# Performance work log

Hardware: AMD Instinct MI355X
Metric: run time of the kernel (lower is better)

The kernel has to match this reference:

```python
import jax, jax.numpy as jnp
import numpy as np

B, N, D, H, MLP_H = 4, 2048, 256, 8, 1024
E = 262144
DH = D // H
EPS = 1e-5

def _ln(x, g, b):
    mu = jnp.mean(x, axis=-1, keepdims=True)
    var = jnp.mean((x - mu) ** 2, axis=-1, keepdims=True)
    return (x - mu) * jax.lax.rsqrt(var + EPS) * g + b

def setup_inputs() -> dict:
    key = jax.random.key(0)
    ks = jax.random.split(key, 16)
    s = 0.02
    return {
        "x": jax.random.normal(ks[0], (B, N, D), jnp.float32),
        "edge_index": jax.random.randint(ks[1], (2, E), 0, B * N, dtype=jnp.int64),
        "gc_w": jax.random.normal(ks[2], (D, D), jnp.float32) * s,
        "gc_b": jnp.zeros((D,), jnp.float32),
        "g_gamma": jnp.ones((D,), jnp.float32), "g_beta": jnp.zeros((D,), jnp.float32),
        "wq": jax.random.normal(ks[3], (D, D), jnp.float32) * s, "bq": jnp.zeros((D,), jnp.float32),
        "wk": jax.random.normal(ks[4], (D, D), jnp.float32) * s, "bk": jnp.zeros((D,), jnp.float32),
        "wv": jax.random.normal(ks[5], (D, D), jnp.float32) * s, "bv": jnp.zeros((D,), jnp.float32),
        "wo": jax.random.normal(ks[6], (D, D), jnp.float32) * s, "bo": jnp.zeros((D,), jnp.float32),
        "a_gamma": jnp.ones((D,), jnp.float32), "a_beta": jnp.zeros((D,), jnp.float32),
        "w1": jax.random.normal(ks[7], (D, MLP_H), jnp.float32) * s, "b1": jnp.zeros((MLP_H,), jnp.float32),
        "w2": jax.random.normal(ks[8], (MLP_H, D), jnp.float32) * s, "b2": jnp.zeros((D,), jnp.float32),
        "m_gamma": jnp.ones((D,), jnp.float32), "m_beta": jnp.zeros((D,), jnp.float32),
    }

def reference(x, edge_index, gc_w, gc_b, g_gamma, g_beta,
              wq, bq, wk, bk, wv, bv, wo, bo, a_gamma, a_beta,
              w1, b1, w2, b2, m_gamma, m_beta):
    BN = B * N
    row, col = edge_index[0], edge_index[1]
    # GraphConvolution with symmetric degree normalization
    xf = x.reshape(BN, D)
    xt = xf @ gc_w  # [BN, D]
    deg = jax.ops.segment_sum(jnp.ones((E,), x.dtype), row, num_segments=BN)
    dis = jnp.where(deg > 0, deg ** -0.5, 0.0)  # deg^-0.5, inf -> 0
    norm = dis[row] * dis[col]  # [E]
    out = jax.ops.segment_sum(norm[:, None] * xt[row], col, num_segments=BN) + gc_b
    x = _ln(x + out.reshape(B, N, D), g_gamma, g_beta)
    # Multi-head self-attention (no mask, dropout=0)
    q = (x @ wq + bq).reshape(B, N, H, DH)
    k = (x @ wk + bk).reshape(B, N, H, DH)
    v = (x @ wv + bv).reshape(B, N, H, DH)
    scores = jnp.einsum("bqhd,bkhd->bhqk", q, k) / jnp.sqrt(jnp.float32(DH))
    attn = jax.nn.softmax(scores, axis=-1)
    ao = jnp.einsum("bhqk,bkhd->bqhd", attn, v).reshape(B, N, D) @ wo + bo
    x = _ln(x + ao, a_gamma, a_beta)
    # MLP (GELU exact, dropout inactive at eval)
    h = jax.nn.gelu(x @ w1 + b1, approximate=False)
    x = _ln(x + (h @ w2 + b2), m_gamma, m_beta)
    return x
```

## Files before the change

kernel.cpp:

```cpp
#include <hip/hip_runtime.h>
#include <math.h>

#define Bb 4
#define Nn 2048
#define Dd 256
#define Hh 8
#define DHh 32
#define MLPH 1024
#define Ee 262144
#define BNr 8192
#define KS_S 40
#define VT_S 72
#define PS 72

typedef __attribute__((ext_vector_type(8))) short bf8;
typedef __attribute__((ext_vector_type(4))) float f4;

__device__ __forceinline__ float gelu_f(float x){
  return 0.5f * x * (1.0f + erff(x * 0.70710678118654752f));
}

__device__ __forceinline__ ushort f2bf(float f){
  union { float f; unsigned u; } v; v.f = f;
  unsigned r = v.u + 0x7fffu + ((v.u >> 16) & 1u);
  return (ushort)(r >> 16);
}
__device__ __forceinline__ float bf2f(ushort u){
  return __uint_as_float((unsigned)u << 16);
}

__global__ void detect_kernel(const int* __restrict__ ei, int* flag){
  __shared__ int nz;
  if (threadIdx.x == 0) nz = 0;
  __syncthreads();
  int any = 0;
  for (int i = threadIdx.x; i < 2048; i += 256)
    if (ei[2*i + 1] != 0) any = 1;
  if (any) atomicOr(&nz, 1);
  __syncthreads();
  if (threadIdx.x == 0) *flag = nz ? 0 : 1;
}

__global__ void count_kernel(const int* __restrict__ ei, const int* __restrict__ flag,
                             int* cnt_row, int* cnt_col){
  int e = blockIdx.x * 256 + threadIdx.x;
  if (e >= Ee) return;
  int m = *flag;
  int r = m ? ei[2*e]          : ei[e];
  int c = m ? ei[2*(Ee + e)]   : ei[Ee + e];
  atomicAdd(&cnt_row[r], 1);
  atomicAdd(&cnt_col[c], 1);
}

__global__ void scan_kernel(const int* __restrict__ cnt, const int* __restrict__ cnt_row,
                            int* start, int* cursor, float* dis){
  __shared__ int part[256];
  int t = threadIdx.x;
  int s = 0;
  for (int i = 0; i < 32; i++) s += cnt[t*32 + i];
  part[t] = s;
  __syncthreads();
  if (t == 0){
    int run = 0;
    for (int i = 0; i < 256; i++){ int tmp = part[i]; part[i] = run; run += tmp; }
    start[BNr] = run;
  }
  __syncthreads();
  int base = part[t];
  for (int i = 0; i < 32; i++){
    start[t*32 + i]  = base;
    cursor[t*32 + i] = base;
    base += cnt[t*32 + i];
  }
  for (int i = t; i < BNr; i += 256){
    int d = cnt_row[i];
    dis[i] = d > 0 ? 1.0f / sqrtf((float)d) : 0.0f;
  }
}

__global__ void fill_kernel(const int* __restrict__ ei, const int* __restrict__ flag,
                            const float* __restrict__ dis,
                            int* cursor, int* bucketR, float* bucketN){
  int e = blockIdx.x * 256 + threadIdx.x;
  if (e >= Ee) return;
  int m = *flag;
  int r = m ? ei[2*e]        : ei[e];
  int c = m ? ei[2*(Ee + e)] : ei[Ee + e];
  int p = atomicAdd(&cursor[c], 1);
  bucketR[p] = r;
  bucketN[p] = dis[r] * dis[c];
}

__global__ void conv_kernel(const float* __restrict__ src, ushort* __restrict__ dst, int n4){
  int i = blockIdx.x * 256 + threadIdx.x;
  if (i < n4){
    float4 v = ((const float4*)src)[i];
    ushort4 o;
    o.x = f2bf(v.x); o.y = f2bf(v.y); o.z = f2bf(v.z); o.w = f2bf(v.w);
    ((ushort4*)dst)[i] = o;
  }
}

__device__ __forceinline__ void tconv_body(const float* src, ushort* dst, int R, int C){
  __shared__ float tile[32][33];
  int c0 = blockIdx.x * 32, r0 = blockIdx.y * 32;
  int tx = threadIdx.x & 31, ty = threadIdx.x >> 5;
  for (int i = ty; i < 32; i += 8)
    tile[i][tx] = src[(size_t)(r0 + i) * C + c0 + tx];
  __syncthreads();
  for (int i = ty; i < 32; i += 8)
    dst[(size_t)(c0 + i) * R + r0 + tx] = f2bf(tile[tx][i]);
}

__global__ void tconv_kernel(const float* __restrict__ src, ushort* __restrict__ dst, int R, int C){
  tconv_body(src, dst, R, C);
}

__global__ void tconv5_kernel(const float* s0, const float* s1, const float* s2,
                              const float* s3, const float* s4,
                              ushort* d0, ushort* d1, ushort* d2, ushort* d3, ushort* d4){
  const float* s; ushort* d;
  switch (blockIdx.z){
    case 0: s = s0; d = d0; break;
    case 1: s = s1; d = d1; break;
    case 2: s = s2; d = d2; break;
    case 3: s = s3; d = d3; break;
    default: s = s4; d = d4; break;
  }
  tconv_body(s, d, 256, 256);
}

__global__ void bias_cat_kernel(const float* __restrict__ bq, const float* __restrict__ bk,
                                const float* __restrict__ bv, float* __restrict__ o){
  int i = blockIdx.x * 256 + threadIdx.x;
  if (i < 256) o[i] = bq[i];
  else if (i < 512) o[i] = bk[i - 256];
  else if (i < 768) o[i] = bv[i - 512];
}

__global__ void vt_kernel(const ushort* __restrict__ Vtmp, ushort* __restrict__ VtG){
  __shared__ ushort tile[32][33];
  int n0 = blockIdx.x * 32, bh = blockIdx.y;
  int b = bh >> 3, h = bh & 7;
  int tx = threadIdx.x & 31, ty = threadIdx.x >> 5;
  for (int i = ty; i < 32; i += 8)
    tile[i][tx] = Vtmp[(size_t)(b*Nn + n0 + i)*Dd + h*DHh + tx];
  __syncthreads();
  for (int i = ty; i < 32; i += 8)
    VtG[(size_t)bh*DHh*Nn + (size_t)i*Nn + n0 + tx] = tile[tx][i];
}

__global__ __launch_bounds__(256) void gather_ln_kernel(
    const ushort* __restrict__ xtb, const int* __restrict__ bucketR,
    const float* __restrict__ bucketN, const int* __restrict__ start,
    const float* __restrict__ x, const float* __restrict__ gc_b,
    const float* __restrict__ gamma, const float* __restrict__ beta,
    float* __restrict__ out, ushort* __restrict__ outb){
  int v = blockIdx.x, t = threadIdx.x;
  int s0 = start[v], s1 = start[v+1];
  float acc = 0.f;
  int ii = s0;
  for (; ii + 1 < s1; ii += 2){
    int   r0 = bucketR[ii],   r1 = bucketR[ii+1];
    float n0 = bucketN[ii],   n1 = bucketN[ii+1];
    float v0 = bf2f(xtb[(size_t)r0*Dd + t]);
    float v1 = bf2f(xtb[(size_t)r1*Dd + t]);
    acc += n0 * v0;
    acc += n1 * v1;
  }
  if (ii < s1){
    acc += bucketN[ii] * bf2f(xtb[(size_t)bucketR[ii]*Dd + t]);
  }
  float val = x[(size_t)v*Dd + t] + acc + gc_b[t];

  float s = val, s2 = val*val;
  #pragma unroll
  for (int o = 32; o > 0; o >>= 1){ s += __shfl_xor(s, o); s2 += __shfl_xor(s2, o); }
  __shared__ float wsA[4], wsB[4];
  int wid = t >> 6, lane = t & 63;
  if (lane == 0){ wsA[wid] = s; wsB[wid] = s2; }
  __syncthreads();
  float mu = (wsA[0]+wsA[1]+wsA[2]+wsA[3]) * (1.0f/Dd);
  float ms = (wsB[0]+wsB[1]+wsB[2]+wsB[3]) * (1.0f/Dd);
  float var = ms - mu*mu;
  float res = (val - mu) * rsqrtf(var + 1e-5f) * gamma[t] + beta[t];
  out[(size_t)v*Dd + t] = res;
  outb[(size_t)v*Dd + t] = f2bf(res);
}

__global__ __launch_bounds__(256) void add_ln_kernel(
    const float* __restrict__ a, const float* __restrict__ b,
    const float* __restrict__ gamma, const float* __restrict__ beta,
    float* __restrict__ out, ushort* __restrict__ outb){
  int row = blockIdx.x, t = threadIdx.x;
  size_t off = (size_t)row*Dd + t;
  float val = a[off] + b[off];

  float s = val, s2 = val*val;
  #pragma unroll
  for (int o = 32; o > 0; o >>= 1){ s += __shfl_xor(s, o); s2 += __shfl_xor(s2, o); }
  __shared__ float wsA[4], wsB[4];
  int wid = t >> 6, lane = t & 63;
  if (lane == 0){ wsA[wid] = s; wsB[wid] = s2; }
  __syncthreads();
  float mu = (wsA[0]+wsA[1]+wsA[2]+wsA[3]) * (1.0f/Dd);
  float ms = (wsB[0]+wsB[1]+wsB[2]+wsB[3]) * (1.0f/Dd);
  float var = ms - mu*mu;
  float res = (val - mu) * rsqrtf(var + 1e-5f) * gamma[t] + beta[t];
  out[off] = res;
  if (outb) outb[off] = f2bf(res);
}

#define LDA_S 56

template<int EPI>
__global__ __launch_bounds__(256,2) void gemm_bf16(
    const ushort* __restrict__ A, const ushort* __restrict__ Bt,
    const float* __restrict__ bias, float* __restrict__ Cf, ushort* __restrict__ Cb,
    int M, int K, int N, float qscale,
    ushort* __restrict__ Qp, ushort* __restrict__ Kp, ushort* __restrict__ Vtmp){
  __shared__ ushort As[2][128*LDA_S];
  __shared__ ushort Bs[2][64*LDA_S];
  int t = threadIdx.x;
  int lane = t & 63, wid = t >> 6;
  int wm = wid >> 1, wn = wid & 1;
  int l15 = lane & 15, lg = lane >> 4;
  int m0 = blockIdx.y * 128, n0 = blockIdx.x * 64;

  int sr = t >> 2;
  int sk = (t & 3) * 8;
  const ushort* Ag1 = A  + (size_t)(m0 + sr) * K + sk;
  const ushort* Ag2 = A  + (size_t)(m0 + 64 + sr) * K + sk;
  const ushort* Bg  = Bt + (size_t)(n0 + sr) * K + sk;

  int nsteps = K / 32;
  bf8 ra1 = *(const bf8*)Ag1;
  bf8 ra2 = *(const bf8*)Ag2;
  bf8 rb  = *(const bf8*)Bg;
  *(bf8*)&As[0][sr*LDA_S + sk]        = ra1;
  *(bf8*)&As[0][(64+sr)*LDA_S + sk]   = ra2;
  *(bf8*)&Bs[0][sr*LDA_S + sk]        = rb;
  __syncthreads();

  f4 acc[4][2] = {};
  for (int ks = 0; ks < nsteps; ks++){
    int cur = ks & 1;
    if (ks + 1 < nsteps){
      ra1 = *(const bf8*)(Ag1 + (ks+1)*32);
      ra2 = *(const bf8*)(Ag2 + (ks+1)*32);
      rb  = *(const bf8*)(Bg  + (ks+1)*32);
    }
    bf8 af[4], bfr[2];
    #pragma unroll
    for (int mf = 0; mf < 4; mf++)
      af[mf] = *(bf8*)&As[cur][(wm*64 + mf*16 + l15)*LDA_S + lg*8];
    #pragma unroll
    for (int nf = 0; nf < 2; nf++)
      bfr[nf] = *(bf8*)&Bs[cur][(wn*32 + nf*16 + l15)*LDA_S + lg*8];
    #pragma unroll
    for (int mf = 0; mf < 4; mf++)
      #pragma unroll
      for (int nf = 0; nf < 2; nf++)
        acc[mf][nf] = __builtin_amdgcn_mfma_f32_16x16x32_bf16(af[mf], bfr[nf], acc[mf][nf], 0, 0, 0);
    __syncthreads();
    if (ks + 1 < nsteps){
      int nxt = cur ^ 1;
      *(bf8*)&As[nxt][sr*LDA_S + sk]      = ra1;
      *(bf8*)&As[nxt][(64+sr)*LDA_S + sk] = ra2;
      *(bf8*)&Bs[nxt][sr*LDA_S + sk]      = rb;
      __syncthreads();
    }
  }

  #pragma unroll
  for (int mf = 0; mf < 4; mf++){
    int row = m0 + wm*64 + mf*16 + lg*4;
    #pragma unroll
    for (int nf = 0; nf < 2; nf++){
      int col = n0 + wn*32 + nf*16 + l15;
      float bv = bias ? bias[col] : 0.f;
      #pragma unroll
      for (int r = 0; r < 4; r++){
        int rr = row + r;
        float v = acc[mf][nf][r] + bv;
        if (EPI == 0){
          Cf[(size_t)rr * N + col] = v;
        } else if (EPI == 2){
          Cb[(size_t)rr * N + col] = f2bf(gelu_f(v));
        } else {
          if (col < 256){
            Qp[(size_t)rr * Dd + col] = f2bf(v * qscale);
          } else if (col < 512){
            int h = (col - 256) >> 5, dh = (col - 256) & 31;
            int bb = rr >> 11, n = rr & 2047;
            Kp[((size_t)(bb*Hh + h)*Nn + n)*DHh + dh] = f2bf(v);
          } else {
            Vtmp[(size_t)rr * Dd + (col - 512)] = f2bf(v);
          }
        }
      }
    }
  }
}

template<int OB>
__global__ __launch_bounds__(256,4) void gemm64_bf16(
    const ushort* __restrict__ A, const ushort* __restrict__ Bt,
    const float* __restrict__ bias, float* __restrict__ Cf, ushort* __restrict__ Cb,
    int M, int K, int N){
  __shared__ ushort As[2][64*LDA_S];
  __shared__ ushort Bs[2][64*LDA_S];
  int t = threadIdx.x;
  int lane = t & 63, wid = t >> 6;
  int wm = wid >> 1, wn = wid & 1;
  int l15 = lane & 15, lg = lane >> 4;
  int m0 = blockIdx.y * 64, n0 = blockIdx.x * 64;
  int sr = t >> 2, sk = (t & 3) * 8;
  const ushort* Ag = A  + (size_t)(m0 + sr) * K + sk;
  const ushort* Bg = Bt + (size_t)(n0 + sr) * K + sk;
  int nsteps = K / 32;
  bf8 ra = *(const bf8*)Ag;
  bf8 rb = *(const bf8*)Bg;
  *(bf8*)&As[0][sr*LDA_S + sk] = ra;
  *(bf8*)&Bs[0][sr*LDA_S + sk] = rb;
  __syncthreads();
  f4 acc[2][2] = {};
  for (int ks = 0; ks < nsteps; ks++){
    int cur = ks & 1;
    if (ks + 1 < nsteps){
      ra = *(const bf8*)(Ag + (ks+1)*32);
      rb = *(const bf8*)(Bg + (ks+1)*32);
    }
    bf8 af[2], bfr[2];
    #pragma unroll
    for (int mf = 0; mf < 2; mf++)
      af[mf] = *(bf8*)&As[cur][(wm*32 + mf*16 + l15)*LDA_S + lg*8];
    #pragma unroll
    for (int nf = 0; nf < 2; nf++)
      bfr[nf] = *(bf8*)&Bs[cur][(wn*32 + nf*16 + l15)*LDA_S + lg*8];
    #pragma unroll
    for (int mf = 0; mf < 2; mf++)
      #pragma unroll
      for (int nf = 0; nf < 2; nf++)
        acc[mf][nf] = __builtin_amdgcn_mfma_f32_16x16x32_bf16(af[mf], bfr[nf], acc[mf][nf], 0, 0, 0);
    __syncthreads();
    if (ks + 1 < nsteps){
      int nxt = cur ^ 1;
      *(bf8*)&As[nxt][sr*LDA_S + sk] = ra;
      *(bf8*)&Bs[nxt][sr*LDA_S + sk] = rb;
      __syncthreads();
    }
  }
  #pragma unroll
  for (int mf = 0; mf < 2; mf++){
    int row = m0 + wm*32 + mf*16 + lg*4;
    #pragma unroll
    for (int nf = 0; nf < 2; nf++){
      int col = n0 + wn*32 + nf*16 + l15;
      float bv = bias ? bias[col] : 0.f;
      #pragma unroll
      for (int r = 0; r < 4; r++){
        float v = acc[mf][nf][r] + bv;
        if (OB) Cb[(size_t)(row + r) * N + col] = f2bf(v);
        else    Cf[(size_t)(row + r) * N + col] = v;
      }
    }
  }
}

__global__ __launch_bounds__(256,2) void attn4_kernel(
    const ushort* __restrict__ Qp, const ushort* __restrict__ Kp,
    const ushort* __restrict__ VtG, ushort* __restrict__ AO){
  __shared__ ushort Ks[2][64*KS_S];
  __shared__ ushort Vt[2][32*VT_S];
  __shared__ ushort Pl[4][32*PS];
  int bh = blockIdx.x >> 4, qb = blockIdx.x & 15;
  int b = bh >> 3, h = bh & 7;
  const ushort* Kh = Kp  + (size_t)bh*Nn*DHh;
  const ushort* Vh = VtG + (size_t)bh*DHh*Nn;
  int t = threadIdx.x;
  int lane = t & 63, wid = t >> 6;
  int l15 = lane & 15, lg = lane >> 4;
  int q0 = qb*128 + wid*32;

  bf8 qf[2];
  #pragma unroll
  for (int mf = 0; mf < 2; mf++)
    qf[mf] = *(const bf8*)&Qp[(size_t)(b*Nn + q0 + mf*16 + l15)*Dd + h*DHh + lg*8];

  int krow = t >> 2, kc8 = (t & 3) * 8;
  int vrow = t >> 3, vc8 = (t & 7) * 8;
  const ushort* Kg = Kh + (size_t)krow*DHh + kc8;
  const ushort* Vg = Vh + (size_t)vrow*Nn + vc8;

  bf8 kreg = *(const bf8*)Kg;
  bf8 vreg = *(const bf8*)Vg;
  *(bf8*)&Ks[0][krow*KS_S + kc8] = kreg;
  *(bf8*)&Vt[0][vrow*VT_S + vc8] = vreg;
  __syncthreads();

  float m_st[2] = {-1e30f, -1e30f};
  float l_st[2] = {0.f, 0.f};
  f4 oacc[2][2] = {};
  ushort* Pw = Pl[wid];

  const int NT = Nn/64;
  for (int kc = 0; kc < NT; kc++){
    int cur = kc & 1;
    if (kc + 1 < NT){
      kreg = *(const bf8*)(Kg + (size_t)(kc+1)*64*DHh);
      vreg = *(const bf8*)(Vg + (kc+1)*64);
    }

    f4 s[4][2] = {};
    #pragma unroll
    for (int kt = 0; kt < 4; kt++){
      bf8 kf = *(bf8*)&Ks[cur][(kt*16 + l15)*KS_S + lg*8];
      #pragma unroll
      for (int mf = 0; mf < 2; mf++)
        s[kt][mf] = __builtin_amdgcn_mfma_f32_16x16x32_bf16(kf, qf[mf], s[kt][mf], 0, 0, 0);
    }

    #pragma unroll
    for (int mf = 0; mf < 2; mf++){
      float mx = s[0][mf][0];
      #pragma unroll
      for (int kt = 0; kt < 4; kt++)
        #pragma unroll
        for (int r = 0; r < 4; r++)
          mx = fmaxf(mx, s[kt][mf][r]);
      if (__any(mx > m_st[mf] + 11.0f)){
        float mw = fmaxf(mx, __shfl_xor(mx, 16));
        mw = fmaxf(mw, __shfl_xor(mw, 32));
        float Mn = fmaxf(m_st[mf], mw);
        float corr = exp2f(m_st[mf] - Mn);
        l_st[mf] *= corr;
        #pragma unroll
        for (int r = 0; r < 4; r++){
          float cr = __shfl(corr, (lane & 48) | (lg*4 + r));
          oacc[mf][0][r] *= cr;
          oacc[mf][1][r] *= cr;
        }
        m_st[mf] = Mn;
      }
      #pragma unroll
      for (int kt = 0; kt < 4; kt++){
        ushort4 pk;
        ushort* pp = (ushort*)&pk;
        #pragma unroll
        for (int r = 0; r < 4; r++){
          float p = exp2f(s[kt][mf][r] - m_st[mf]);
          unsigned pb = __float_as_uint(p) & 0xffff0000u;
          pp[r] = (ushort)(pb >> 16);
          l_st[mf] += __uint_as_float(pb);
        }
        *(ushort4*)&Pw[(mf*16 + l15)*PS + kt*16 + lg*4] = pk;
      }
    }

    #pragma unroll
    for (int mf = 0; mf < 2; mf++)
      #pragma unroll
      for (int ksb = 0; ksb < 2; ksb++){
        bf8 pf = *(bf8*)&Pw[(mf*16 + l15)*PS + ksb*32 + lg*8];
        #pragma unroll
        for (int nt = 0; nt < 2; nt++){
          bf8 vf = *(bf8*)&Vt[cur][(nt*16 + l15)*VT_S + ksb*32 + lg*8];
          oacc[mf][nt] = __builtin_amdgcn_mfma_f32_16x16x32_bf16(pf, vf, oacc[mf][nt], 0, 0, 0);
        }
      }

    if (kc + 1 < NT){
      *(bf8*)&Ks[cur^1][krow*KS_S + kc8] = kreg;
      *(bf8*)&Vt[cur^1][vrow*VT_S + vc8] = vreg;
    }
    __syncthreads();
  }

  #pragma unroll
  for (int mf = 0; mf < 2; mf++){
    float l = l_st[mf];
    l += __shfl_xor(l, 16);
    l += __shfl_xor(l, 32);
    float invl = 1.0f / l;
    #pragma unroll
    for (int r = 0; r < 4; r++){
      float il = __shfl(invl, (lane & 48) | (lg*4 + r));
      int row = b*Nn + q0 + mf*16 + lg*4 + r;
      #pragma unroll
      for (int nt = 0; nt < 2; nt++)
        AO[(size_t)row*Dd + h*DHh + nt*16 + l15] = f2bf(oacc[mf][nt][r] * il);
    }
  }
}

extern "C" void kernel_launch(void* const* d_in, const int* in_sizes, int n_in,
                              void* d_out, int out_size, void* d_ws, size_t ws_size,
                              hipStream_t stream){
  const float* x      = (const float*)d_in[0];
  const int*   ei     = (const int*)d_in[1];
  const float* gc_w   = (const float*)d_in[2];
  const float* gc_b   = (const float*)d_in[3];
  const float* g_gamma= (const float*)d_in[4];
  const float* g_beta = (const float*)d_in[5];
  const float* wq = (const float*)d_in[6];  const float* bq = (const float*)d_in[7];
  const float* wk = (const float*)d_in[8];  const float* bk = (const float*)d_in[9];
  const float* wv = (const float*)d_in[10]; const float* bv = (const float*)d_in[11];
  const float* wo = (const float*)d_in[12]; const float* bo = (const float*)d_in[13];
  const float* a_gamma = (const float*)d_in[14]; const float* a_beta = (const float*)d_in[15];
  const float* w1 = (const float*)d_in[16]; const float* b1 = (const float*)d_in[17];
  const float* w2 = (const float*)d_in[18]; const float* b2 = (const float*)d_in[19];
  const float* m_gamma = (const float*)d_in[20]; const float* m_beta = (const float*)d_in[21];
  float* out = (float*)d_out;

  const size_t S = (size_t)BNr * Dd;

  char* p = (char*)d_ws;
  auto alloc = [&](size_t bytes){ char* r = p; p += (bytes + 255) & ~(size_t)255; return r; };

  float* X1    = (float*)alloc(S * 4);
  float* X2    = (float*)alloc(S * 4);
  float* MO    = (float*)alloc(S * 4);
  float* PROJ  = (float*)alloc(S * 4);
  ushort* Qp   = (ushort*)alloc(S * 2);
  ushort* Kp   = (ushort*)alloc(S * 2);
  ushort* Vtmp = (ushort*)alloc(S * 2);
  ushort* VtG  = (ushort*)alloc(S * 2);
  ushort* regA = (ushort*)alloc(S * 2);
  ushort* regB = (ushort*)alloc(S * 2);
  ushort* X1b  = (ushort*)alloc(S * 2);
  ushort* Hb   = (ushort*)alloc((size_t)BNr * MLPH * 2);
  ushort* gcwT = (ushort*)alloc(65536 * 2);
  ushort* wqkvT= (ushort*)alloc(196608 * 2);
  ushort* woT  = (ushort*)alloc(65536 * 2);
  ushort* w1T  = (ushort*)alloc(262144 * 2);
  ushort* w2T  = (ushort*)alloc(262144 * 2);
  float* bqkv  = (float*)alloc(768 * 4);
  int* cnt_row = (int*)alloc(8192 * 4);
  int* cnt_col = (int*)alloc(8192 * 4);
  int* startA  = (int*)alloc(8200 * 4);
  int* cursor  = (int*)alloc(8192 * 4);
  int* bucketR = (int*)alloc(Ee * 4);
  float* bucketN = (float*)alloc(Ee * 4);
  float* dis   = (float*)alloc(8192 * 4);
  int* flag    = (int*)alloc(256);

  ushort* xbf = regA;  ushort* AOb = regA;
  ushort* XTb = regB;  ushort* X2b = regB;

  hipMemsetAsync(cnt_row, 0, 8192 * sizeof(int), stream);
  hipMemsetAsync(cnt_col, 0, 8192 * sizeof(int), stream);

  detect_kernel<<<1, 256, 0, stream>>>(ei, flag);
  count_kernel<<<Ee/256, 256, 0, stream>>>(ei, flag, cnt_row, cnt_col);
  scan_kernel<<<1, 256, 0, stream>>>(cnt_col, cnt_row, startA, cursor, dis);
  fill_kernel<<<Ee/256, 256, 0, stream>>>(ei, flag, dis, cursor, bucketR, bucketN);

  conv_kernel<<<(int)(S/4/256), 256, 0, stream>>>(x, xbf, (int)(S/4));
  tconv5_kernel<<<dim3(8,8,5), 256, 0, stream>>>(gc_w, wq, wk, wv, wo,
      gcwT, wqkvT, wqkvT + 65536, wqkvT + 131072, woT);
  tconv_kernel<<<dim3(32,8), 256, 0, stream>>>(w1, w1T, 256, 1024);
  tconv_kernel<<<dim3(8,32), 256, 0, stream>>>(w2, w2T, 1024, 256);
  bias_cat_kernel<<<3, 256, 0, stream>>>(bq, bk, bv, bqkv);

  const float qscale = 0.17677669529663687f * 1.4426950408889634f;

  gemm64_bf16<1><<<dim3(Dd/64, BNr/64), 256, 0, stream>>>(
      xbf, gcwT, nullptr, nullptr, XTb, BNr, Dd, Dd);
  gather_ln_kernel<<<BNr, 256, 0, stream>>>(XTb, bucketR, bucketN, startA,
                                            x, gc_b, g_gamma, g_beta, X1, X1b);
  gemm_bf16<3><<<dim3(768/64, BNr/128), 256, 0, stream>>>(
      X1b, wqkvT, bqkv, nullptr, nullptr, BNr, Dd, 768, qscale, Qp, Kp, Vtmp);
  vt_kernel<<<dim3(Nn/32, Bb*Hh), 256, 0, stream>>>(Vtmp, VtG);
  attn4_kernel<<<Bb*Hh*16, 256, 0, stream>>>(Qp, Kp, VtG, AOb);
  gemm64_bf16<0><<<dim3(Dd/64, BNr/64), 256, 0, stream>>>(
      AOb, woT, bo, PROJ, nullptr, BNr, Dd, Dd);
  add_ln_kernel<<<BNr, 256, 0, stream>>>(X1, PROJ, a_gamma, a_beta, X2, X2b);
  gemm_bf16<2><<<dim3(MLPH/64, BNr/128), 256, 0, stream>>>(
      X2b, w1T, b1, nullptr, Hb, BNr, Dd, MLPH, 1.0f, nullptr, nullptr, nullptr);
  gemm64_bf16<0><<<dim3(Dd/64, BNr/64), 256, 0, stream>>>(
      Hb, w2T, b2, MO, nullptr, BNr, MLPH, Dd);
  add_ln_kernel<<<BNr, 256, 0, stream>>>(X2, MO, m_gamma, m_beta, out, nullptr);
}
```

Baseline: 357.1 us.

## Fuse conversions and V transpose, keep attention P in registers, pack edge buckets

Several separate changes land together. The x-to-bf16 conversion is folded into the first GEMM's A-load, and the V transpose kernel is dropped because the QKV GEMM epilogue writes V already transposed. Edge row and norm are packed into one int2 bucket, and the gather loop is unrolled by four. The attention kernel now uses 16 query rows per wave and feeds P straight from registers into 16x16x16 MFMAs with no LDS round trip, and the two memsets are merged into one. These cut kernel launches, global traffic and LDS traffic. In exchange the attention kernel does less MFMA work per K/V tile loaded and runs twice as many blocks.

```diff
diff --git a/kernel.cpp b/kernel.cpp
--- a/kernel.cpp
+++ b/kernel.cpp
@@ -11,9 +11,9 @@
 #define BNr 8192
 #define KS_S 40
 #define VT_S 72
-#define PS 72
 
 typedef __attribute__((ext_vector_type(8))) short bf8;
+typedef __attribute__((ext_vector_type(4))) short s4v;
 typedef __attribute__((ext_vector_type(4))) float f4;
 
 __device__ __forceinline__ float gelu_f(float x){
@@ -80,25 +80,17 @@
 
 __global__ void fill_kernel(const int* __restrict__ ei, const int* __restrict__ flag,
                             const float* __restrict__ dis,
-                            int* cursor, int* bucketR, float* bucketN){
+                            int* cursor, int2* bucket){
   int e = blockIdx.x * 256 + threadIdx.x;
   if (e >= Ee) return;
   int m = *flag;
   int r = m ? ei[2*e]        : ei[e];
   int c = m ? ei[2*(Ee + e)] : ei[Ee + e];
   int p = atomicAdd(&cursor[c], 1);
-  bucketR[p] = r;
-  bucketN[p] = dis[r] * dis[c];
-}
-
-__global__ void conv_kernel(const float* __restrict__ src, ushort* __restrict__ dst, int n4){
-  int i = blockIdx.x * 256 + threadIdx.x;
-  if (i < n4){
-    float4 v = ((const float4*)src)[i];
-    ushort4 o;
-    o.x = f2bf(v.x); o.y = f2bf(v.y); o.z = f2bf(v.z); o.w = f2bf(v.w);
-    ((ushort4*)dst)[i] = o;
-  }
+  int2 pk;
+  pk.x = r;
+  pk.y = __float_as_int(dis[r] * dis[c]);
+  bucket[p] = pk;
 }
 
 __device__ __forceinline__ void tconv_body(const float* src, ushort* dst, int R, int C){
@@ -138,21 +130,9 @@
   else if (i < 768) o[i] = bv[i - 512];
 }
 
-__global__ void vt_kernel(const ushort* __restrict__ Vtmp, ushort* __restrict__ VtG){
-  __shared__ ushort tile[32][33];
-  int n0 = blockIdx.x * 32, bh = blockIdx.y;
-  int b = bh >> 3, h = bh & 7;
-  int tx = threadIdx.x & 31, ty = threadIdx.x >> 5;
-  for (int i = ty; i < 32; i += 8)
-    tile[i][tx] = Vtmp[(size_t)(b*Nn + n0 + i)*Dd + h*DHh + tx];
-  __syncthreads();
-  for (int i = ty; i < 32; i += 8)
-    VtG[(size_t)bh*DHh*Nn + (size_t)i*Nn + n0 + tx] = tile[tx][i];
-}
-
 __global__ __launch_bounds__(256) void gather_ln_kernel(
-    const ushort* __restrict__ xtb, const int* __restrict__ bucketR,
-    const float* __restrict__ bucketN, const int* __restrict__ start,
+    const ushort* __restrict__ xtb, const int2* __restrict__ bucket,
+    const int* __restrict__ start,
     const float* __restrict__ x, const float* __restrict__ gc_b,
     const float* __restrict__ gamma, const float* __restrict__ beta,
     float* __restrict__ out, ushort* __restrict__ outb){
@@ -160,16 +140,19 @@
   int s0 = start[v], s1 = start[v+1];
   float acc = 0.f;
   int ii = s0;
-  for (; ii + 1 < s1; ii += 2){
-    int   r0 = bucketR[ii],   r1 = bucketR[ii+1];
-    float n0 = bucketN[ii],   n1 = bucketN[ii+1];
-    float v0 = bf2f(xtb[(size_t)r0*Dd + t]);
-    float v1 = bf2f(xtb[(size_t)r1*Dd + t]);
-    acc += n0 * v0;
-    acc += n1 * v1;
-  }
-  if (ii < s1){
-    acc += bucketN[ii] * bf2f(xtb[(size_t)bucketR[ii]*Dd + t]);
+  for (; ii + 3 < s1; ii += 4){
+    int2 e0 = bucket[ii],   e1 = bucket[ii+1];
+    int2 e2 = bucket[ii+2], e3 = bucket[ii+3];
+    float v0 = bf2f(xtb[(size_t)e0.x*Dd + t]);
+    float v1 = bf2f(xtb[(size_t)e1.x*Dd + t]);
+    float v2 = bf2f(xtb[(size_t)e2.x*Dd + t]);
+    float v3 = bf2f(xtb[(size_t)e3.x*Dd + t]);
+    acc += __int_as_float(e0.y) * v0 + __int_as_float(e1.y) * v1;
+    acc += __int_as_float(e2.y) * v2 + __int_as_float(e3.y) * v3;
+  }
+  for (; ii < s1; ii++){
+    int2 e = bucket[ii];
+    acc += __int_as_float(e.y) * bf2f(xtb[(size_t)e.x*Dd + t]);
   }
   float val = x[(size_t)v*Dd + t] + acc + gc_b[t];
 
@@ -218,7 +201,7 @@
     const ushort* __restrict__ A, const ushort* __restrict__ Bt,
     const float* __restrict__ bias, float* __restrict__ Cf, ushort* __restrict__ Cb,
     int M, int K, int N, float qscale,
-    ushort* __restrict__ Qp, ushort* __restrict__ Kp, ushort* __restrict__ Vtmp){
+    ushort* __restrict__ Qp, ushort* __restrict__ Kp, ushort* __restrict__ VtG){
   __shared__ ushort As[2][128*LDA_S];
   __shared__ ushort Bs[2][64*LDA_S];
   int t = threadIdx.x;
@@ -279,33 +262,42 @@
     for (int nf = 0; nf < 2; nf++){
       int col = n0 + wn*32 + nf*16 + l15;
       float bv = bias ? bias[col] : 0.f;
-      #pragma unroll
-      for (int r = 0; r < 4; r++){
-        int rr = row + r;
-        float v = acc[mf][nf][r] + bv;
-        if (EPI == 0){
-          Cf[(size_t)rr * N + col] = v;
-        } else if (EPI == 2){
-          Cb[(size_t)rr * N + col] = f2bf(gelu_f(v));
+      float vv[4];
+      #pragma unroll
+      for (int r = 0; r < 4; r++) vv[r] = acc[mf][nf][r] + bv;
+      if (EPI == 0){
+        #pragma unroll
+        for (int r = 0; r < 4; r++) Cf[(size_t)(row + r) * N + col] = vv[r];
+      } else if (EPI == 2){
+        #pragma unroll
+        for (int r = 0; r < 4; r++) Cb[(size_t)(row + r) * N + col] = f2bf(gelu_f(vv[r]));
+      } else {
+        if (n0 < 256){
+          #pragma unroll
+          for (int r = 0; r < 4; r++)
+            Qp[(size_t)(row + r) * Dd + col] = f2bf(vv[r] * qscale);
+        } else if (n0 < 512){
+          int h = (col - 256) >> 5, dh = (col - 256) & 31;
+          int bb = row >> 11, n = row & 2047;
+          #pragma unroll
+          for (int r = 0; r < 4; r++)
+            Kp[((size_t)(bb*Hh + h)*Nn + n + r)*DHh + dh] = f2bf(vv[r]);
         } else {
-          if (col < 256){
-            Qp[(size_t)rr * Dd + col] = f2bf(v * qscale);
-          } else if (col < 512){
-            int h = (col - 256) >> 5, dh = (col - 256) & 31;
-            int bb = rr >> 11, n = rr & 2047;
-            Kp[((size_t)(bb*Hh + h)*Nn + n)*DHh + dh] = f2bf(v);
-          } else {
-            Vtmp[(size_t)rr * Dd + (col - 512)] = f2bf(v);
-          }
+          int h = (col - 512) >> 5, dh = (col - 512) & 31;
+          int bb = row >> 11, n = row & 2047;
+          ushort4 pk;
+          pk.x = f2bf(vv[0]); pk.y = f2bf(vv[1]);
+          pk.z = f2bf(vv[2]); pk.w = f2bf(vv[3]);
+          *(ushort4*)&VtG[((size_t)(bb*Hh + h)*DHh + dh)*Nn + n] = pk;
         }
       }
     }
   }
 }
 
-template<int OB>
+template<int OB, int AF>
 __global__ __launch_bounds__(256,4) void gemm64_bf16(
-    const ushort* __restrict__ A, const ushort* __restrict__ Bt,
+    const void* __restrict__ Av, const ushort* __restrict__ Bt,
     const float* __restrict__ bias, float* __restrict__ Cf, ushort* __restrict__ Cb,
     int M, int K, int N){
   __shared__ ushort As[2][64*LDA_S];
@@ -316,19 +308,32 @@
   int l15 = lane & 15, lg = lane >> 4;
   int m0 = blockIdx.y * 64, n0 = blockIdx.x * 64;
   int sr = t >> 2, sk = (t & 3) * 8;
-  const ushort* Ag = A  + (size_t)(m0 + sr) * K + sk;
+  const ushort* Ag = (const ushort*)Av + (size_t)(m0 + sr) * K + sk;
+  const float*  Af = (const float*)Av  + (size_t)(m0 + sr) * K + sk;
   const ushort* Bg = Bt + (size_t)(n0 + sr) * K + sk;
   int nsteps = K / 32;
-  bf8 ra = *(const bf8*)Ag;
+
+  bf8 ra; float4 rf0, rf1;
+  if (AF){ rf0 = *(const float4*)Af; rf1 = *(const float4*)(Af + 4); }
+  else   { ra = *(const bf8*)Ag; }
   bf8 rb = *(const bf8*)Bg;
-  *(bf8*)&As[0][sr*LDA_S + sk] = ra;
+  if (AF){
+    bf8 c;
+    c[0]=(short)f2bf(rf0.x); c[1]=(short)f2bf(rf0.y); c[2]=(short)f2bf(rf0.z); c[3]=(short)f2bf(rf0.w);
+    c[4]=(short)f2bf(rf1.x); c[5]=(short)f2bf(rf1.y); c[6]=(short)f2bf(rf1.z); c[7]=(short)f2bf(rf1.w);
+    *(bf8*)&As[0][sr*LDA_S + sk] = c;
+  } else {
+    *(bf8*)&As[0][sr*LDA_S + sk] = ra;
+  }
   *(bf8*)&Bs[0][sr*LDA_S + sk] = rb;
   __syncthreads();
+
   f4 acc[2][2] = {};
   for (int ks = 0; ks < nsteps; ks++){
     int cur = ks & 1;
     if (ks + 1 < nsteps){
-      ra = *(const bf8*)(Ag + (ks+1)*32);
+      if (AF){ rf0 = *(const float4*)(Af + (ks+1)*32); rf1 = *(const float4*)(Af + (ks+1)*32 + 4); }
+      else   { ra = *(const bf8*)(Ag + (ks+1)*32); }
       rb = *(const bf8*)(Bg + (ks+1)*32);
     }
     bf8 af[2], bfr[2];
@@ -346,7 +351,14 @@
     __syncthreads();
     if (ks + 1 < nsteps){
       int nxt = cur ^ 1;
-      *(bf8*)&As[nxt][sr*LDA_S + sk] = ra;
+      if (AF){
+        bf8 c;
+        c[0]=(short)f2bf(rf0.x); c[1]=(short)f2bf(rf0.y); c[2]=(short)f2bf(rf0.z); c[3]=(short)f2bf(rf0.w);
+        c[4]=(short)f2bf(rf1.x); c[5]=(short)f2bf(rf1.y); c[6]=(short)f2bf(rf1.z); c[7]=(short)f2bf(rf1.w);
+        *(bf8*)&As[nxt][sr*LDA_S + sk] = c;
+      } else {
+        *(bf8*)&As[nxt][sr*LDA_S + sk] = ra;
+      }
       *(bf8*)&Bs[nxt][sr*LDA_S + sk] = rb;
       __syncthreads();
     }
@@ -368,25 +380,21 @@
   }
 }
 
-__global__ __launch_bounds__(256,2) void attn4_kernel(
+__global__ __launch_bounds__(256,4) void attn5_kernel(
     const ushort* __restrict__ Qp, const ushort* __restrict__ Kp,
     const ushort* __restrict__ VtG, ushort* __restrict__ AO){
   __shared__ ushort Ks[2][64*KS_S];
   __shared__ ushort Vt[2][32*VT_S];
-  __shared__ ushort Pl[4][32*PS];
-  int bh = blockIdx.x >> 4, qb = blockIdx.x & 15;
+  int bh = blockIdx.x >> 5, qb = blockIdx.x & 31;
   int b = bh >> 3, h = bh & 7;
   const ushort* Kh = Kp  + (size_t)bh*Nn*DHh;
   const ushort* Vh = VtG + (size_t)bh*DHh*Nn;
   int t = threadIdx.x;
   int lane = t & 63, wid = t >> 6;
   int l15 = lane & 15, lg = lane >> 4;
-  int q0 = qb*128 + wid*32;
-
-  bf8 qf[2];
-  #pragma unroll
-  for (int mf = 0; mf < 2; mf++)
-    qf[mf] = *(const bf8*)&Qp[(size_t)(b*Nn + q0 + mf*16 + l15)*Dd + h*DHh + lg*8];
+  int q0 = qb*64 + wid*16;
+
+  bf8 qf = *(const bf8*)&Qp[(size_t)(b*Nn + q0 + l15)*Dd + h*DHh + lg*8];
 
   int krow = t >> 2, kc8 = (t & 3) * 8;
   int vrow = t >> 3, vc8 = (t & 7) * 8;
@@ -399,10 +407,8 @@
   *(bf8*)&Vt[0][vrow*VT_S + vc8] = vreg;
   __syncthreads();
 
-  float m_st[2] = {-1e30f, -1e30f};
-  float l_st[2] = {0.f, 0.f};
-  f4 oacc[2][2] = {};
-  ushort* Pw = Pl[wid];
+  float m_st = -1e30f, l_st = 0.f;
+  f4 oacc[2] = {};
 
   const int NT = Nn/64;
   for (int kc = 0; kc < NT; kc++){
@@ -412,62 +418,60 @@
       vreg = *(const bf8*)(Vg + (kc+1)*64);
     }
 
-    f4 s[4][2] = {};
+    f4 s[4] = {};
     #pragma unroll
     for (int kt = 0; kt < 4; kt++){
       bf8 kf = *(bf8*)&Ks[cur][(kt*16 + l15)*KS_S + lg*8];
-      #pragma unroll
-      for (int mf = 0; mf < 2; mf++)
-        s[kt][mf] = __builtin_amdgcn_mfma_f32_16x16x32_bf16(kf, qf[mf], s[kt][mf], 0, 0, 0);
-    }
-
-    #pragma unroll
-    for (int mf = 0; mf < 2; mf++){
-      float mx = s[0][mf][0];
-      #pragma unroll
-      for (int kt = 0; kt < 4; kt++)
-        #pragma unroll
-        for (int r = 0; r < 4; r++)
-          mx = fmaxf(mx, s[kt][mf][r]);
-      if (__any(mx > m_st[mf] + 11.0f)){
-        float mw = fmaxf(mx, __shfl_xor(mx, 16));
-        mw = fmaxf(mw, __shfl_xor(mw, 32));
-        float Mn = fmaxf(m_st[mf], mw);
-        float corr = exp2f(m_st[mf] - Mn);
-        l_st[mf] *= corr;
-        #pragma unroll
-        for (int r = 0; r < 4; r++){
-          float cr = __shfl(corr, (lane & 48) | (lg*4 + r));
-          oacc[mf][0][r] *= cr;
-          oacc[mf][1][r] *= cr;
-        }
-        m_st[mf] = Mn;
+      s[kt] = __builtin_amdgcn_mfma_f32_16x16x32_bf16(kf, qf, s[kt], 0, 0, 0);
+    }
+
+    float mx = s[0][0];
+    #pragma unroll
+    for (int kt = 0; kt < 4; kt++)
+      #pragma unroll
+      for (int r = 0; r < 4; r++)
+        mx = fmaxf(mx, s[kt][r]);
+    if (__any(mx > m_st + 11.0f)){
+      float mw = fmaxf(mx, __shfl_xor(mx, 16));
+      mw = fmaxf(mw, __shfl_xor(mw, 32));
+      float Mn = fmaxf(m_st, mw);
+      float corr = exp2f(m_st - Mn);
+      l_st *= corr;
+      #pragma unroll
+      for (int r = 0; r < 4; r++){
+        float cr = __shfl(corr, (lane & 48) | (lg*4 + r));
+        oacc[0][r] *= cr;
+        oacc[1][r] *= cr;
       }
-      #pragma unroll
-      for (int kt = 0; kt < 4; kt++){
-        ushort4 pk;
-        ushort* pp = (ushort*)&pk;
-        #pragma unroll
-        for (int r = 0; r < 4; r++){
-          float p = exp2f(s[kt][mf][r] - m_st[mf]);
-          unsigned pb = __float_as_uint(p) & 0xffff0000u;
-          pp[r] = (ushort)(pb >> 16);
-          l_st[mf] += __uint_as_float(pb);
-        }
-        *(ushort4*)&Pw[(mf*16 + l15)*PS + kt*16 + lg*4] = pk;
+      m_st = Mn;
+    }
+
+    s4v pa[4];
+    float ps = 0.f;
+    #pragma unroll
+    for (int kt = 0; kt < 4; kt++){
+      unsigned pb[4];
+      #pragma unroll
+      for (int r = 0; r < 4; r++){
+        float p = exp2f(s[kt][r] - m_st);
+        pb[r] = __float_as_uint(p) & 0xffff0000u;
+        ps += __uint_as_float(pb[r]);
       }
-    }
-
-    #pragma unroll
-    for (int mf = 0; mf < 2; mf++)
-      #pragma unroll
-      for (int ksb = 0; ksb < 2; ksb++){
-        bf8 pf = *(bf8*)&Pw[(mf*16 + l15)*PS + ksb*32 + lg*8];
-        #pragma unroll
-        for (int nt = 0; nt < 2; nt++){
-          bf8 vf = *(bf8*)&Vt[cur][(nt*16 + l15)*VT_S + ksb*32 + lg*8];
-          oacc[mf][nt] = __builtin_amdgcn_mfma_f32_16x16x32_bf16(pf, vf, oacc[mf][nt], 0, 0, 0);
-        }
+      union { unsigned u[2]; s4v v; } cvt;
+      cvt.u[0] = (pb[0] >> 16) | pb[1];
+      cvt.u[1] = (pb[2] >> 16) | pb[3];
+      pa[kt] = cvt.v;
+    }
+    ps += __shfl_xor(ps, 16);
+    ps += __shfl_xor(ps, 32);
+    l_st += ps;
+
+    #pragma unroll
+    for (int kt = 0; kt < 4; kt++)
+      #pragma unroll
+      for (int nt = 0; nt < 2; nt++){
+        s4v vf = *(const s4v*)&Vt[cur][(nt*16 + l15)*VT_S + kt*16 + lg*4];
+        oacc[nt] = __builtin_amdgcn_mfma_f32_16x16x16bf16_1k(pa[kt], vf, oacc[nt], 0, 0, 0);
       }
 
     if (kc + 1 < NT){
@@ -477,20 +481,17 @@
     __syncthreads();
   }
 
+  float l = l_st;
+  l += __shfl_xor(l, 16);
+  l += __shfl_xor(l, 32);
+  float invl = 1.0f / l;
   #pragma unroll
-  for (int mf = 0; mf < 2; mf++){
-    float l = l_st[mf];
-    l += __shfl_xor(l, 16);
-    l += __shfl_xor(l, 32);
-    float invl = 1.0f / l;
-    #pragma unroll
-    for (int r = 0; r < 4; r++){
-      float il = __shfl(invl, (lane & 48) | (lg*4 + r));
-      int row = b*Nn + q0 + mf*16 + lg*4 + r;
-      #pragma unroll
-      for (int nt = 0; nt < 2; nt++)
-        AO[(size_t)row*Dd + h*DHh + nt*16 + l15] = f2bf(oacc[mf][nt][r] * il);
-    }
+  for (int r = 0; r < 4; r++){
+    float il = __shfl(invl, (lane & 48) | (lg*4 + r));
+    int row = b*Nn + q0 + lg*4 + r;
+    #pragma unroll
+    for (int nt = 0; nt < 2; nt++)
+      AO[(size_t)row*Dd + h*DHh + nt*16 + l15] = f2bf(oacc[nt][r] * il);
   }
 }
 
@@ -524,10 +525,9 @@
   float* PROJ  = (float*)alloc(S * 4);
   ushort* Qp   = (ushort*)alloc(S * 2);
   ushort* Kp   = (ushort*)alloc(S * 2);
-  ushort* Vtmp = (ushort*)alloc(S * 2);
   ushort* VtG  = (ushort*)alloc(S * 2);
   ushort* regA = (ushort*)alloc(S * 2);
-  ushort* regB = (ushort*)alloc(S * 2);
+  ushort* XTb  = (ushort*)alloc(S * 2);
   ushort* X1b  = (ushort*)alloc(S * 2);
   ushort* Hb   = (ushort*)alloc((size_t)BNr * MLPH * 2);
   ushort* gcwT = (ushort*)alloc(65536 * 2);
@@ -540,23 +540,20 @@
   int* cnt_col = (int*)alloc(8192 * 4);
   int* startA  = (int*)alloc(8200 * 4);
   int* cursor  = (int*)alloc(8192 * 4);
-  int* bucketR = (int*)alloc(Ee * 4);
-  float* bucketN = (float*)alloc(Ee * 4);
+  int2* bucket = (int2*)alloc(Ee * 8);
   float* dis   = (float*)alloc(8192 * 4);
   int* flag    = (int*)alloc(256);
 
-  ushort* xbf = regA;  ushort* AOb = regA;
-  ushort* XTb = regB;  ushort* X2b = regB;
-
-  hipMemsetAsync(cnt_row, 0, 8192 * sizeof(int), stream);
-  hipMemsetAsync(cnt_col, 0, 8192 * sizeof(int), stream);
+  ushort* AOb = regA;
+  ushort* X2b = XTb;
+
+  hipMemsetAsync(cnt_row, 0, 2 * 8192 * sizeof(int), stream);
 
   detect_kernel<<<1, 256, 0, stream>>>(ei, flag);
   count_kernel<<<Ee/256, 256, 0, stream>>>(ei, flag, cnt_row, cnt_col);
   scan_kernel<<<1, 256, 0, stream>>>(cnt_col, cnt_row, startA, cursor, dis);
-  fill_kernel<<<Ee/256, 256, 0, stream>>>(ei, flag, dis, cursor, bucketR, bucketN);
-
-  conv_kernel<<<(int)(S/4/256), 256, 0, stream>>>(x, xbf, (int)(S/4));
+  fill_kernel<<<Ee/256, 256, 0, stream>>>(ei, flag, dis, cursor, bucket);
+
   tconv5_kernel<<<dim3(8,8,5), 256, 0, stream>>>(gc_w, wq, wk, wv, wo,
       gcwT, wqkvT, wqkvT + 65536, wqkvT + 131072, woT);
   tconv_kernel<<<dim3(32,8), 256, 0, stream>>>(w1, w1T, 256, 1024);
@@ -565,20 +562,19 @@
 
   const float qscale = 0.17677669529663687f * 1.4426950408889634f;
 
-  gemm64_bf16<1><<<dim3(Dd/64, BNr/64), 256, 0, stream>>>(
-      xbf, gcwT, nullptr, nullptr, XTb, BNr, Dd, Dd);
-  gather_ln_kernel<<<BNr, 256, 0, stream>>>(XTb, bucketR, bucketN, startA,
+  gemm64_bf16<1,1><<<dim3(Dd/64, BNr/64), 256, 0, stream>>>(
+      x, gcwT, nullptr, nullptr, XTb, BNr, Dd, Dd);
+  gather_ln_kernel<<<BNr, 256, 0, stream>>>(XTb, bucket, startA,
                                             x, gc_b, g_gamma, g_beta, X1, X1b);
   gemm_bf16<3><<<dim3(768/64, BNr/128), 256, 0, stream>>>(
-      X1b, wqkvT, bqkv, nullptr, nullptr, BNr, Dd, 768, qscale, Qp, Kp, Vtmp);
-  vt_kernel<<<dim3(Nn/32, Bb*Hh), 256, 0, stream>>>(Vtmp, VtG);
-  attn4_kernel<<<Bb*Hh*16, 256, 0, stream>>>(Qp, Kp, VtG, AOb);
-  gemm64_bf16<0><<<dim3(Dd/64, BNr/64), 256, 0, stream>>>(
+      X1b, wqkvT, bqkv, nullptr, nullptr, BNr, Dd, 768, qscale, Qp, Kp, VtG);
+  attn5_kernel<<<Bb*Hh*32, 256, 0, stream>>>(Qp, Kp, VtG, AOb);
+  gemm64_bf16<0,0><<<dim3(Dd/64, BNr/64), 256, 0, stream>>>(
       AOb, woT, bo, PROJ, nullptr, BNr, Dd, Dd);
   add_ln_kernel<<<BNr, 256, 0, stream>>>(X1, PROJ, a_gamma, a_beta, X2, X2b);
   gemm_bf16<2><<<dim3(MLPH/64, BNr/128), 256, 0, stream>>>(
       X2b, w1T, b1, nullptr, Hb, BNr, Dd, MLPH, 1.0f, nullptr, nullptr, nullptr);
-  gemm64_bf16<0><<<dim3(Dd/64, BNr/64), 256, 0, stream>>>(
+  gemm64_bf16<0,0><<<dim3(Dd/64, BNr/64), 256, 0, stream>>>(
       Hb, w2T, b2, MO, nullptr, BNr, MLPH, Dd);
   add_ln_kernel<<<BNr, 256, 0, stream>>>(X2, MO, m_gamma, m_beta, out, nullptr);
 }
```

Measured after the change: 341.6 us. -4.3%, faster.
